# Kernel optimization log

Hardware: AMD Instinct MI355X
Metric: run time of the kernel (lower is better)

Reference implementation:

```python
import jax, jax.numpy as jnp
import numpy as np

N_NODES = 1_000_000
MEM_DIM = 128
MSG_DIM = 256
N_UPD = 200_000


def setup_inputs() -> dict:
    key = jax.random.key(0)
    k0, k1, k2, k3, k4 = jax.random.split(key, 5)
    memory = jax.random.normal(k0, (N_NODES, MEM_DIM), dtype=jnp.float32)
    last_update = jnp.zeros((N_NODES,), dtype=jnp.float32)
    # 'unique' node ids: arange guarantees uniqueness and in-range values
    unique_node_ids = jnp.arange(N_UPD, dtype=jnp.int32)
    unique_messages = jax.random.normal(k1, (N_UPD, MSG_DIM), dtype=jnp.float32)
    timestamps = jax.random.uniform(k2, (N_UPD,), dtype=jnp.float32) * 1000.0
    # torch.nn.GRUCell parameters (the TGN memory_updater)
    scale = 1.0 / np.sqrt(MEM_DIM)
    W_ih = jax.random.uniform(k3, (3 * MEM_DIM, MSG_DIM), jnp.float32, -scale, scale)
    W_hh = jax.random.uniform(k4, (3 * MEM_DIM, MEM_DIM), jnp.float32, -scale, scale)
    b_ih = jnp.zeros((3 * MEM_DIM,), jnp.float32)
    b_hh = jnp.zeros((3 * MEM_DIM,), jnp.float32)
    return {
        "memory": memory,
        "last_update": last_update,
        "unique_node_ids": unique_node_ids,
        "unique_messages": unique_messages,
        "timestamps": timestamps,
        "W_ih": W_ih,
        "W_hh": W_hh,
        "b_ih": b_ih,
        "b_hh": b_hh,
    }


def _gru_cell(x, h, W_ih, W_hh, b_ih, b_hh):
    # torch.nn.GRUCell math
    gi = x @ W_ih.T + b_ih          # [U, 3H]
    gh = h @ W_hh.T + b_hh          # [U, 3H]
    i_r, i_z, i_n = jnp.split(gi, 3, axis=-1)
    h_r, h_z, h_n = jnp.split(gh, 3, axis=-1)
    r = jax.nn.sigmoid(i_r + h_r)
    z = jax.nn.sigmoid(i_z + h_z)
    n = jnp.tanh(i_n + r * h_n)
    return (1.0 - z) * n + z * h


def reference(memory, last_update, unique_node_ids, unique_messages, timestamps,
              W_ih, W_hh, b_ih, b_hh):
    # gather rows of the node memory (get_memory / updated_memory[unique_node_ids])
    h = memory[unique_node_ids]                              # [U, H]
    new_h = _gru_cell(unique_messages, h, W_ih, W_hh, b_ih, b_hh)
    # scatter updated rows back (set_memory) and update timestamps
    updated_memory = memory.at[unique_node_ids].set(new_h)
    updated_last_update = last_update.at[unique_node_ids].set(timestamps)
    return updated_memory, updated_last_update
```

## Files before the change

kernel.cpp:

```cpp
#include <hip/hip_runtime.h>
#include <hip/hip_bf16.h>
#include <stdint.h>

#define MEM_DIM 128
#define MSG_DIM 256
#define KTOT    384
#define BM      64

typedef __attribute__((ext_vector_type(8))) __bf16 bf16x8;
typedef __attribute__((ext_vector_type(4))) float  f32x4;

union B8u { uint32_t u[4]; bf16x8 v; };

__device__ __forceinline__ uint32_t cvt_pk(float lo, float hi) {
    uint32_t r;
    asm("v_cvt_pk_bf16_f32 %0, %1, %2" : "=v"(r) : "v"(lo), "v"(hi));
    return r;
}

__device__ __forceinline__ bf16x8 load_cvt8(const float* __restrict__ p) {
    f32x4 a = *(const f32x4*)p;
    f32x4 b = *(const f32x4*)(p + 4);
    B8u r;
    r.u[0] = cvt_pk(a.x, a.y);
    r.u[1] = cvt_pk(a.z, a.w);
    r.u[2] = cvt_pk(b.x, b.y);
    r.u[3] = cvt_pk(b.z, b.w);
    return r.v;
}

__device__ __forceinline__ float sigm(float x) {
    return __builtin_amdgcn_rcpf(1.0f + __expf(-x));
}
__device__ __forceinline__ float tanh_fast(float x) {
    return 1.0f - 2.0f * __builtin_amdgcn_rcpf(1.0f + __expf(2.0f * x));
}

__global__ void bm_zero_kernel(uint32_t* __restrict__ bm, int nwords) {
    int i = blockIdx.x * 256 + threadIdx.x;
    if (i < nwords) bm[i] = 0;
}
__global__ void bm_set_kernel(const int* __restrict__ ids, uint32_t* __restrict__ bm, int U) {
    int i = blockIdx.x * 256 + threadIdx.x;
    if (i < U) {
        int id = ids[i];
        atomicOr(&bm[id >> 5], 1u << (id & 31));
    }
}

__global__ void wconv_kernel(const float* __restrict__ wih,
                             const float* __restrict__ whh,
                             __hip_bfloat16* __restrict__ out) {
    int i = blockIdx.x * 256 + threadIdx.x;
    const int NIH = 3 * MEM_DIM * MSG_DIM;
    const int NHH = 3 * MEM_DIM * MEM_DIM;
    if (i < NIH)            out[i] = __float2bfloat16(wih[i]);
    else if (i < NIH + NHH) out[i] = __float2bfloat16(whh[i - NIH]);
}

__global__ void copy_skip_kernel(const f32x4* __restrict__ mem,
                                 const float* __restrict__ lu,
                                 f32x4* __restrict__ outm,
                                 float* __restrict__ outlu,
                                 const uint32_t* __restrict__ bm,
                                 int NN) {
    const int64_t n_mem_chunks = (int64_t)NN * 32;
    const int64_t total = n_mem_chunks + NN;
    const int64_t stride = (int64_t)gridDim.x * blockDim.x;
    for (int64_t i = (int64_t)blockIdx.x * blockDim.x + threadIdx.x; i < total; i += stride) {
        if (i < n_mem_chunks) {
            int row = (int)(i >> 5);
            if (!((bm[row >> 5] >> (row & 31)) & 1u)) {
                f32x4 v = __builtin_nontemporal_load(&mem[i]);
                __builtin_nontemporal_store(v, &outm[i]);
            }
        } else {
            int node = (int)(i - n_mem_chunks);
            if (!((bm[node >> 5] >> (node & 31)) & 1u))
                outlu[node] = lu[node];
        }
    }
}

__global__ void copy_all_kernel(const f32x4* __restrict__ mem,
                                const f32x4* __restrict__ lu,
                                f32x4* __restrict__ out,
                                int n_mem4, int n_tot4) {
    int stride = gridDim.x * blockDim.x;
    for (int i = blockIdx.x * blockDim.x + threadIdx.x; i < n_tot4; i += stride) {
        f32x4 v = (i < n_mem4) ? mem[i]
                               : __builtin_nontemporal_load(&lu[i - n_mem4]);
        __builtin_nontemporal_store(v, &out[i]);
    }
}

__device__ __forceinline__ int at_addr(int row, int kbyte) {
    return (row * (KTOT * 2) + kbyte) ^ ((row & 7) << 4);
}

template<bool PRE>
__global__ __launch_bounds__(512, 4)
void gru_stream_kernel(const float* __restrict__ memory,
                       const int*   __restrict__ ids,
                       const float* __restrict__ msgs,
                       const float* __restrict__ ts,
                       const float* __restrict__ Wih,
                       const float* __restrict__ Whh,
                       const float* __restrict__ bih,
                       const float* __restrict__ bhh,
                       const __hip_bfloat16* __restrict__ WihB,
                       const __hip_bfloat16* __restrict__ WhhB,
                       float* __restrict__ out_mem,
                       float* __restrict__ out_lu,
                       int U) {
    __shared__ __align__(16) char At[BM * KTOT * 2];

    const int tid  = threadIdx.x;
    const int w    = tid >> 6;
    const int lane = tid & 63;
    const int lq   = lane & 15;
    const int lk   = lane >> 4;
    const int rb   = blockIdx.x * BM;

    if (tid < BM) {
        int r = rb + tid;
        if (r < U) out_lu[ids[r]] = ts[r];
    }

    {
        int r = tid >> 3, seg = tid & 7;
        int rA = rb + r; if (rA >= U) rA = U - 1;
        const float* xp = msgs + (size_t)rA * MSG_DIM + seg * 32;
        #pragma unroll
        for (int i = 0; i < 4; ++i)
            *(bf16x8*)(At + at_addr(r, seg * 64 + i * 16)) = load_cvt8(xp + i * 8);
    }
    {
        int r = tid >> 3, u = tid & 7;
        int rA = rb + r; if (rA >= U) rA = U - 1;
        const float* hp = memory + (size_t)ids[rA] * MEM_DIM + u * 16;
        *(bf16x8*)(At + at_addr(r, 512 + u * 32))      = load_cvt8(hp);
        *(bf16x8*)(At + at_addr(r, 512 + u * 32 + 16)) = load_cvt8(hp + 8);
    }

    const int c = w * 16 + lq;
    const float br  = bih[c] + bhh[c];
    const float bz  = bih[MEM_DIM + c] + bhh[MEM_DIM + c];
    const float bin = bih[2 * MEM_DIM + c];
    const float bhn = bhh[2 * MEM_DIM + c];

    const __hip_bfloat16* wih_l = WihB + c * MSG_DIM + lk * 8;
    const __hip_bfloat16* whh_l = WhhB + c * MEM_DIM + lk * 8;
    const float* wih_f = Wih + c * MSG_DIM + lk * 8;
    const float* whh_f = Whh + c * MEM_DIM + lk * 8;

    const f32x4 z4 = {0.f, 0.f, 0.f, 0.f};
    f32x4 acc[4][4];
    #pragma unroll
    for (int m = 0; m < 4; ++m)
        #pragma unroll
        for (int q = 0; q < 4; ++q) acc[m][q] = z4;

    __syncthreads();

    #pragma unroll 1
    for (int ks = 0; ks < 8; ++ks) {
        bf16x8 bv0, bv1, bv2;
        if (PRE) {
            bv0 = *(const bf16x8*)(wih_l + 0 * 128 * MSG_DIM + ks * 32);
            bv1 = *(const bf16x8*)(wih_l + 1 * 128 * MSG_DIM + ks * 32);
            bv2 = *(const bf16x8*)(wih_l + 2 * 128 * MSG_DIM + ks * 32);
        } else {
            bv0 = load_cvt8(wih_f + 0 * 128 * MSG_DIM + ks * 32);
            bv1 = load_cvt8(wih_f + 1 * 128 * MSG_DIM + ks * 32);
            bv2 = load_cvt8(wih_f + 2 * 128 * MSG_DIM + ks * 32);
        }
        bf16x8 af[4];
        #pragma unroll
        for (int m = 0; m < 4; ++m)
            af[m] = *(const bf16x8*)(At + at_addr(m * 16 + lq, ks * 64 + lk * 16));
        #pragma unroll
        for (int m = 0; m < 4; ++m)
            acc[m][0] = __builtin_amdgcn_mfma_f32_16x16x32_bf16(af[m], bv0, acc[m][0], 0, 0, 0);
        #pragma unroll
        for (int m = 0; m < 4; ++m)
            acc[m][1] = __builtin_amdgcn_mfma_f32_16x16x32_bf16(af[m], bv1, acc[m][1], 0, 0, 0);
        #pragma unroll
        for (int m = 0; m < 4; ++m)
            acc[m][2] = __builtin_amdgcn_mfma_f32_16x16x32_bf16(af[m], bv2, acc[m][2], 0, 0, 0);
    }
    #pragma unroll 1
    for (int ks = 0; ks < 4; ++ks) {
        bf16x8 bv0, bv1, bv2;
        if (PRE) {
            bv0 = *(const bf16x8*)(whh_l + 0 * 128 * MEM_DIM + ks * 32);
            bv1 = *(const bf16x8*)(whh_l + 1 * 128 * MEM_DIM + ks * 32);
            bv2 = *(const bf16x8*)(whh_l + 2 * 128 * MEM_DIM + ks * 32);
        } else {
            bv0 = load_cvt8(whh_f + 0 * 128 * MEM_DIM + ks * 32);
            bv1 = load_cvt8(whh_f + 1 * 128 * MEM_DIM + ks * 32);
            bv2 = load_cvt8(whh_f + 2 * 128 * MEM_DIM + ks * 32);
        }
        bf16x8 af[4];
        #pragma unroll
        for (int m = 0; m < 4; ++m)
            af[m] = *(const bf16x8*)(At + at_addr(m * 16 + lq, 512 + ks * 64 + lk * 16));
        #pragma unroll
        for (int m = 0; m < 4; ++m)
            acc[m][0] = __builtin_amdgcn_mfma_f32_16x16x32_bf16(af[m], bv0, acc[m][0], 0, 0, 0);
        #pragma unroll
        for (int m = 0; m < 4; ++m)
            acc[m][1] = __builtin_amdgcn_mfma_f32_16x16x32_bf16(af[m], bv1, acc[m][1], 0, 0, 0);
        #pragma unroll
        for (int m = 0; m < 4; ++m)
            acc[m][3] = __builtin_amdgcn_mfma_f32_16x16x32_bf16(af[m], bv2, acc[m][3], 0, 0, 0);
    }

    #pragma unroll
    for (int m = 0; m < 4; ++m) {
        #pragma unroll
        for (int j = 0; j < 4; ++j) {
            int row = m * 16 + lk * 4 + j;
            int r = rb + row;
            if (r < U) {
                int id = ids[r];
                float hold = __bfloat162float(
                    *(const __hip_bfloat16*)(At + at_addr(row, 512 + c * 2)));
                float rg = sigm(acc[m][0][j] + br);
                float zg = sigm(acc[m][1][j] + bz);
                float ng = tanh_fast(acc[m][2][j] + bin + rg * (acc[m][3][j] + bhn));
                out_mem[(size_t)id * MEM_DIM + c] = (1.0f - zg) * ng + zg * hold;
            }
        }
    }
}

extern "C" void kernel_launch(void* const* d_in, const int* in_sizes, int n_in,
                              void* d_out, int out_size, void* d_ws, size_t ws_size,
                              hipStream_t stream) {
    const float* memory      = (const float*)d_in[0];
    const float* last_update = (const float*)d_in[1];
    const int*   ids         = (const int*)  d_in[2];
    const float* msgs        = (const float*)d_in[3];
    const float* ts          = (const float*)d_in[4];
    const float* Wih         = (const float*)d_in[5];
    const float* Whh         = (const float*)d_in[6];
    const float* bih         = (const float*)d_in[7];
    const float* bhh         = (const float*)d_in[8];

    const int NN = in_sizes[1];
    const int U  = in_sizes[2];

    float* out_mem = (float*)d_out;
    float* out_lu  = out_mem + (size_t)NN * MEM_DIM;

    const int NIH = 3 * MEM_DIM * MSG_DIM;
    const int NHH = 3 * MEM_DIM * MEM_DIM;
    const size_t WBYTES  = (size_t)(NIH + NHH) * sizeof(__hip_bfloat16);
    const size_t BM_OFF  = (WBYTES + 255) & ~(size_t)255;
    const int    BMWORDS = (NN + 31) / 32;
    const int    nblocks = (U + BM - 1) / BM;

    if (ws_size >= BM_OFF + (size_t)BMWORDS * 4) {
        __hip_bfloat16* wb = (__hip_bfloat16*)d_ws;
        uint32_t* bm = (uint32_t*)((char*)d_ws + BM_OFF);

        wconv_kernel<<<(NIH + NHH + 255) / 256, 256, 0, stream>>>(Wih, Whh, wb);
        bm_zero_kernel<<<(BMWORDS + 255) / 256, 256, 0, stream>>>(bm, BMWORDS);
        bm_set_kernel<<<(U + 255) / 256, 256, 0, stream>>>(ids, bm, U);

        gru_stream_kernel<true><<<nblocks, 512, 0, stream>>>(
            memory, ids, msgs, ts, Wih, Whh, bih, bhh,
            wb, wb + NIH, out_mem, out_lu, U);

        copy_skip_kernel<<<8192, 256, 0, stream>>>((const f32x4*)memory, last_update,
                                                   (f32x4*)out_mem, out_lu, bm, NN);
    } else {
        int n_mem4 = NN * MEM_DIM / 4;
        int n_tot4 = n_mem4 + NN / 4;
        copy_all_kernel<<<8192, 256, 0, stream>>>((const f32x4*)memory,
                                                  (const f32x4*)last_update,
                                                  (f32x4*)d_out, n_mem4, n_tot4);
        gru_stream_kernel<false><<<nblocks, 512, 0, stream>>>(
            memory, ids, msgs, ts, Wih, Whh, bih, bhh,
            nullptr, nullptr, out_mem, out_lu, U);
    }
}
```

Before: 353.4 us.

## Make GRU kernel persistent over tiles and merge weight-conversion with bitmap zeroing

```diff
diff --git a/kernel.cpp b/kernel.cpp
--- a/kernel.cpp
+++ b/kernel.cpp
@@ -36,9 +36,16 @@
     return 1.0f - 2.0f * __builtin_amdgcn_rcpf(1.0f + __expf(2.0f * x));
 }
 
-__global__ void bm_zero_kernel(uint32_t* __restrict__ bm, int nwords) {
+__global__ void init_kernel(const float* __restrict__ wih,
+                            const float* __restrict__ whh,
+                            __hip_bfloat16* __restrict__ wb,
+                            uint32_t* __restrict__ bm, int bmwords) {
     int i = blockIdx.x * 256 + threadIdx.x;
-    if (i < nwords) bm[i] = 0;
+    const int NIH = 3 * MEM_DIM * MSG_DIM;
+    const int NHH = 3 * MEM_DIM * MEM_DIM;
+    if (i < NIH)            wb[i] = __float2bfloat16(wih[i]);
+    else if (i < NIH + NHH) wb[i] = __float2bfloat16(whh[i - NIH]);
+    if (i < bmwords) bm[i] = 0;
 }
 __global__ void bm_set_kernel(const int* __restrict__ ids, uint32_t* __restrict__ bm, int U) {
     int i = blockIdx.x * 256 + threadIdx.x;
@@ -46,16 +53,6 @@
         int id = ids[i];
         atomicOr(&bm[id >> 5], 1u << (id & 31));
     }
-}
-
-__global__ void wconv_kernel(const float* __restrict__ wih,
-                             const float* __restrict__ whh,
-                             __hip_bfloat16* __restrict__ out) {
-    int i = blockIdx.x * 256 + threadIdx.x;
-    const int NIH = 3 * MEM_DIM * MSG_DIM;
-    const int NHH = 3 * MEM_DIM * MEM_DIM;
-    if (i < NIH)            out[i] = __float2bfloat16(wih[i]);
-    else if (i < NIH + NHH) out[i] = __float2bfloat16(whh[i - NIH]);
 }
 
 __global__ void copy_skip_kernel(const f32x4* __restrict__ mem,
@@ -100,19 +97,19 @@
 
 template<bool PRE>
 __global__ __launch_bounds__(512, 4)
-void gru_stream_kernel(const float* __restrict__ memory,
-                       const int*   __restrict__ ids,
-                       const float* __restrict__ msgs,
-                       const float* __restrict__ ts,
-                       const float* __restrict__ Wih,
-                       const float* __restrict__ Whh,
-                       const float* __restrict__ bih,
-                       const float* __restrict__ bhh,
-                       const __hip_bfloat16* __restrict__ WihB,
-                       const __hip_bfloat16* __restrict__ WhhB,
-                       float* __restrict__ out_mem,
-                       float* __restrict__ out_lu,
-                       int U) {
+void gru_persist_kernel(const float* __restrict__ memory,
+                        const int*   __restrict__ ids,
+                        const float* __restrict__ msgs,
+                        const float* __restrict__ ts,
+                        const float* __restrict__ Wih,
+                        const float* __restrict__ Whh,
+                        const float* __restrict__ bih,
+                        const float* __restrict__ bhh,
+                        const __hip_bfloat16* __restrict__ WihB,
+                        const __hip_bfloat16* __restrict__ WhhB,
+                        float* __restrict__ out_mem,
+                        float* __restrict__ out_lu,
+                        int U, int ntiles) {
     __shared__ __align__(16) char At[BM * KTOT * 2];
 
     const int tid  = threadIdx.x;
@@ -120,28 +117,6 @@
     const int lane = tid & 63;
     const int lq   = lane & 15;
     const int lk   = lane >> 4;
-    const int rb   = blockIdx.x * BM;
-
-    if (tid < BM) {
-        int r = rb + tid;
-        if (r < U) out_lu[ids[r]] = ts[r];
-    }
-
-    {
-        int r = tid >> 3, seg = tid & 7;
-        int rA = rb + r; if (rA >= U) rA = U - 1;
-        const float* xp = msgs + (size_t)rA * MSG_DIM + seg * 32;
-        #pragma unroll
-        for (int i = 0; i < 4; ++i)
-            *(bf16x8*)(At + at_addr(r, seg * 64 + i * 16)) = load_cvt8(xp + i * 8);
-    }
-    {
-        int r = tid >> 3, u = tid & 7;
-        int rA = rb + r; if (rA >= U) rA = U - 1;
-        const float* hp = memory + (size_t)ids[rA] * MEM_DIM + u * 16;
-        *(bf16x8*)(At + at_addr(r, 512 + u * 32))      = load_cvt8(hp);
-        *(bf16x8*)(At + at_addr(r, 512 + u * 32 + 16)) = load_cvt8(hp + 8);
-    }
 
     const int c = w * 16 + lq;
     const float br  = bih[c] + bhh[c];
@@ -155,81 +130,111 @@
     const float* whh_f = Whh + c * MEM_DIM + lk * 8;
 
     const f32x4 z4 = {0.f, 0.f, 0.f, 0.f};
-    f32x4 acc[4][4];
-    #pragma unroll
-    for (int m = 0; m < 4; ++m)
-        #pragma unroll
-        for (int q = 0; q < 4; ++q) acc[m][q] = z4;
-
-    __syncthreads();
 
     #pragma unroll 1
-    for (int ks = 0; ks < 8; ++ks) {
-        bf16x8 bv0, bv1, bv2;
-        if (PRE) {
-            bv0 = *(const bf16x8*)(wih_l + 0 * 128 * MSG_DIM + ks * 32);
-            bv1 = *(const bf16x8*)(wih_l + 1 * 128 * MSG_DIM + ks * 32);
-            bv2 = *(const bf16x8*)(wih_l + 2 * 128 * MSG_DIM + ks * 32);
-        } else {
-            bv0 = load_cvt8(wih_f + 0 * 128 * MSG_DIM + ks * 32);
-            bv1 = load_cvt8(wih_f + 1 * 128 * MSG_DIM + ks * 32);
-            bv2 = load_cvt8(wih_f + 2 * 128 * MSG_DIM + ks * 32);
-        }
-        bf16x8 af[4];
+    for (int t = blockIdx.x; t < ntiles; t += gridDim.x) {
+        const int rb = t * BM;
+
+        if (t != (int)blockIdx.x)
+            __syncthreads();
+
+        if (tid < BM) {
+            int r = rb + tid;
+            if (r < U) out_lu[ids[r]] = ts[r];
+        }
+
+        {
+            int r = tid >> 3, seg = tid & 7;
+            int rA = rb + r; if (rA >= U) rA = U - 1;
+            const float* xp = msgs + (size_t)rA * MSG_DIM + seg * 32;
+            #pragma unroll
+            for (int i = 0; i < 4; ++i)
+                *(bf16x8*)(At + at_addr(r, seg * 64 + i * 16)) = load_cvt8(xp + i * 8);
+        }
+        {
+            int r = tid >> 3, u = tid & 7;
+            int rA = rb + r; if (rA >= U) rA = U - 1;
+            const float* hp = memory + (size_t)ids[rA] * MEM_DIM + u * 16;
+            *(bf16x8*)(At + at_addr(r, 512 + u * 32))      = load_cvt8(hp);
+            *(bf16x8*)(At + at_addr(r, 512 + u * 32 + 16)) = load_cvt8(hp + 8);
+        }
+
+        f32x4 acc[4][4];
         #pragma unroll
         for (int m = 0; m < 4; ++m)
-            af[m] = *(const bf16x8*)(At + at_addr(m * 16 + lq, ks * 64 + lk * 16));
+            #pragma unroll
+            for (int q = 0; q < 4; ++q) acc[m][q] = z4;
+
+        __syncthreads();
+
+        #pragma unroll 1
+        for (int ks = 0; ks < 8; ++ks) {
+            bf16x8 bv0, bv1, bv2;
+            if (PRE) {
+                bv0 = *(const bf16x8*)(wih_l + 0 * 128 * MSG_DIM + ks * 32);
+                bv1 = *(const bf16x8*)(wih_l + 1 * 128 * MSG_DIM + ks * 32);
+                bv2 = *(const bf16x8*)(wih_l + 2 * 128 * MSG_DIM + ks * 32);
+            } else {
+                bv0 = load_cvt8(wih_f + 0 * 128 * MSG_DIM + ks * 32);
+                bv1 = load_cvt8(wih_f + 1 * 128 * MSG_DIM + ks * 32);
+                bv2 = load_cvt8(wih_f + 2 * 128 * MSG_DIM + ks * 32);
+            }
+            bf16x8 af[4];
+            #pragma unroll
+            for (int m = 0; m < 4; ++m)
+                af[m] = *(const bf16x8*)(At + at_addr(m * 16 + lq, ks * 64 + lk * 16));
+            #pragma unroll
+            for (int m = 0; m < 4; ++m)
+                acc[m][0] = __builtin_amdgcn_mfma_f32_16x16x32_bf16(af[m], bv0, acc[m][0], 0, 0, 0);
+            #pragma unroll
+            for (int m = 0; m < 4; ++m)
+                acc[m][1] = __builtin_amdgcn_mfma_f32_16x16x32_bf16(af[m], bv1, acc[m][1], 0, 0, 0);
+            #pragma unroll
+            for (int m = 0; m < 4; ++m)
+                acc[m][2] = __builtin_amdgcn_mfma_f32_16x16x32_bf16(af[m], bv2, acc[m][2], 0, 0, 0);
+        }
+        #pragma unroll 1
+        for (int ks = 0; ks < 4; ++ks) {
+            bf16x8 bv0, bv1, bv2;
+            if (PRE) {
+                bv0 = *(const bf16x8*)(whh_l + 0 * 128 * MEM_DIM + ks * 32);
+                bv1 = *(const bf16x8*)(whh_l + 1 * 128 * MEM_DIM + ks * 32);
+                bv2 = *(const bf16x8*)(whh_l + 2 * 128 * MEM_DIM + ks * 32);
+            } else {
+                bv0 = load_cvt8(whh_f + 0 * 128 * MEM_DIM + ks * 32);
+                bv1 = load_cvt8(whh_f + 1 * 128 * MEM_DIM + ks * 32);
+                bv2 = load_cvt8(whh_f + 2 * 128 * MEM_DIM + ks * 32);
+            }
+            bf16x8 af[4];
+            #pragma unroll
+            for (int m = 0; m < 4; ++m)
+                af[m] = *(const bf16x8*)(At + at_addr(m * 16 + lq, 512 + ks * 64 + lk * 16));
+            #pragma unroll
+            for (int m = 0; m < 4; ++m)
+                acc[m][0] = __builtin_amdgcn_mfma_f32_16x16x32_bf16(af[m], bv0, acc[m][0], 0, 0, 0);
+            #pragma unroll
+            for (int m = 0; m < 4; ++m)
+                acc[m][1] = __builtin_amdgcn_mfma_f32_16x16x32_bf16(af[m], bv1, acc[m][1], 0, 0, 0);
+            #pragma unroll
+            for (int m = 0; m < 4; ++m)
+                acc[m][3] = __builtin_amdgcn_mfma_f32_16x16x32_bf16(af[m], bv2, acc[m][3], 0, 0, 0);
+        }
+
         #pragma unroll
-        for (int m = 0; m < 4; ++m)
-            acc[m][0] = __builtin_amdgcn_mfma_f32_16x16x32_bf16(af[m], bv0, acc[m][0], 0, 0, 0);
-        #pragma unroll
-        for (int m = 0; m < 4; ++m)
-            acc[m][1] = __builtin_amdgcn_mfma_f32_16x16x32_bf16(af[m], bv1, acc[m][1], 0, 0, 0);
-        #pragma unroll
-        for (int m = 0; m < 4; ++m)
-            acc[m][2] = __builtin_amdgcn_mfma_f32_16x16x32_bf16(af[m], bv2, acc[m][2], 0, 0, 0);
-    }
-    #pragma unroll 1
-    for (int ks = 0; ks < 4; ++ks) {
-        bf16x8 bv0, bv1, bv2;
-        if (PRE) {
-            bv0 = *(const bf16x8*)(whh_l + 0 * 128 * MEM_DIM + ks * 32);
-            bv1 = *(const bf16x8*)(whh_l + 1 * 128 * MEM_DIM + ks * 32);
-            bv2 = *(const bf16x8*)(whh_l + 2 * 128 * MEM_DIM + ks * 32);
-        } else {
-            bv0 = load_cvt8(whh_f + 0 * 128 * MEM_DIM + ks * 32);
-            bv1 = load_cvt8(whh_f + 1 * 128 * MEM_DIM + ks * 32);
-            bv2 = load_cvt8(whh_f + 2 * 128 * MEM_DIM + ks * 32);
-        }
-        bf16x8 af[4];
-        #pragma unroll
-        for (int m = 0; m < 4; ++m)
-            af[m] = *(const bf16x8*)(At + at_addr(m * 16 + lq, 512 + ks * 64 + lk * 16));
-        #pragma unroll
-        for (int m = 0; m < 4; ++m)
-            acc[m][0] = __builtin_amdgcn_mfma_f32_16x16x32_bf16(af[m], bv0, acc[m][0], 0, 0, 0);
-        #pragma unroll
-        for (int m = 0; m < 4; ++m)
-            acc[m][1] = __builtin_amdgcn_mfma_f32_16x16x32_bf16(af[m], bv1, acc[m][1], 0, 0, 0);
-        #pragma unroll
-        for (int m = 0; m < 4; ++m)
-            acc[m][3] = __builtin_amdgcn_mfma_f32_16x16x32_bf16(af[m], bv2, acc[m][3], 0, 0, 0);
-    }
-
-    #pragma unroll
-    for (int m = 0; m < 4; ++m) {
-        #pragma unroll
-        for (int j = 0; j < 4; ++j) {
-            int row = m * 16 + lk * 4 + j;
-            int r = rb + row;
-            if (r < U) {
-                int id = ids[r];
-                float hold = __bfloat162float(
-                    *(const __hip_bfloat16*)(At + at_addr(row, 512 + c * 2)));
-                float rg = sigm(acc[m][0][j] + br);
-                float zg = sigm(acc[m][1][j] + bz);
-                float ng = tanh_fast(acc[m][2][j] + bin + rg * (acc[m][3][j] + bhn));
-                out_mem[(size_t)id * MEM_DIM + c] = (1.0f - zg) * ng + zg * hold;
+        for (int m = 0; m < 4; ++m) {
+            #pragma unroll
+            for (int j = 0; j < 4; ++j) {
+                int row = m * 16 + lk * 4 + j;
+                int r = rb + row;
+                if (r < U) {
+                    int id = ids[r];
+                    float hold = __bfloat162float(
+                        *(const __hip_bfloat16*)(At + at_addr(row, 512 + c * 2)));
+                    float rg = sigm(acc[m][0][j] + br);
+                    float zg = sigm(acc[m][1][j] + bz);
+                    float ng = tanh_fast(acc[m][2][j] + bin + rg * (acc[m][3][j] + bhn));
+                    out_mem[(size_t)id * MEM_DIM + c] = (1.0f - zg) * ng + zg * hold;
+                }
             }
         }
     }
@@ -259,19 +264,20 @@
     const size_t WBYTES  = (size_t)(NIH + NHH) * sizeof(__hip_bfloat16);
     const size_t BM_OFF  = (WBYTES + 255) & ~(size_t)255;
     const int    BMWORDS = (NN + 31) / 32;
-    const int    nblocks = (U + BM - 1) / BM;
+    const int    ntiles  = (U + BM - 1) / BM;
+    const int    GRID    = (ntiles < 768) ? ntiles : 768;
 
     if (ws_size >= BM_OFF + (size_t)BMWORDS * 4) {
         __hip_bfloat16* wb = (__hip_bfloat16*)d_ws;
         uint32_t* bm = (uint32_t*)((char*)d_ws + BM_OFF);
 
-        wconv_kernel<<<(NIH + NHH + 255) / 256, 256, 0, stream>>>(Wih, Whh, wb);
-        bm_zero_kernel<<<(BMWORDS + 255) / 256, 256, 0, stream>>>(bm, BMWORDS);
+        int initn = (NIH + NHH > BMWORDS) ? (NIH + NHH) : BMWORDS;
+        init_kernel<<<(initn + 255) / 256, 256, 0, stream>>>(Wih, Whh, wb, bm, BMWORDS);
         bm_set_kernel<<<(U + 255) / 256, 256, 0, stream>>>(ids, bm, U);
 
-        gru_stream_kernel<true><<<nblocks, 512, 0, stream>>>(
+        gru_persist_kernel<true><<<GRID, 512, 0, stream>>>(
             memory, ids, msgs, ts, Wih, Whh, bih, bhh,
-            wb, wb + NIH, out_mem, out_lu, U);
+            wb, wb + NIH, out_mem, out_lu, U, ntiles);
 
         copy_skip_kernel<<<8192, 256, 0, stream>>>((const f32x4*)memory, last_update,
                                                    (f32x4*)out_mem, out_lu, bm, NN);
@@ -281,8 +287,8 @@
         copy_all_kernel<<<8192, 256, 0, stream>>>((const f32x4*)memory,
                                                   (const f32x4*)last_update,
                                                   (f32x4*)d_out, n_mem4, n_tot4);
-        gru_stream_kernel<false><<<nblocks, 512, 0, stream>>>(
+        gru_persist_kernel<false><<<GRID, 512, 0, stream>>>(
             memory, ids, msgs, ts, Wih, Whh, bih, bhh,
-            nullptr, nullptr, out_mem, out_lu, U);
-    }
-}
+            nullptr, nullptr, out_mem, out_lu, U, ntiles);
+    }
+}
```

New measurement: 407.3 us. +15.2%, slower.
